# Kernel tuning notes

Hardware: AMD Instinct MI355X
Metric: run time of the kernel (lower is better)

Reference implementation:

```python
import jax, jax.numpy as jnp
import numpy as np

B, S, D, H = 4, 1024, 1024, 16
HD = D // H
NEG = 10000.0


def setup_inputs() -> dict:
    key = jax.random.key(0)
    k1, k2, k3 = jax.random.split(key, 3)
    std = 0.02
    return {
        "x": jax.random.normal(k1, (B, S, D), dtype=jnp.float32),
        "mask": jnp.zeros((B, 1, 1, S), dtype=jnp.float32),
        "w_attn": jax.random.normal(k2, (D, 3 * D), dtype=jnp.float32) * std,
        "b_attn": jnp.zeros((1, 3 * D), dtype=jnp.float32),
        "w_proj": jax.random.normal(k3, (D, D), dtype=jnp.float32) * std,
        "b_proj": jnp.zeros((1, D), dtype=jnp.float32),
    }


def reference(x, mask, w_attn, b_attn, w_proj, b_proj):
    b, s, d = x.shape
    # fused QKV projection (Conv1D == dense over last dim)
    qkv = x @ w_attn + b_attn  # [B,S,3D]
    q, k, v = jnp.split(qkv, 3, axis=2)

    def split_heads(t):  # [B,S,D] -> [B,H,S,HD]
        return t.reshape(b, s, H, HD).transpose(0, 2, 1, 3)

    q, k, v = split_heads(q), split_heads(k), split_heads(v)

    w = jnp.einsum("bhqd,bhkd->bhqk", q, k) / jnp.sqrt(jnp.float32(HD))
    # causal mask (lower triangle from lower-right corner)
    i = jnp.arange(s)[:, None]
    j = jnp.arange(s)[None, :]
    bmask = (i >= j).astype(w.dtype)[None, None]  # [1,1,S,S]
    w = w * bmask - NEG * (1.0 - bmask)
    w = w + mask
    w = jax.nn.softmax(w, axis=-1)  # attn_dropout is identity at inference
    a = jnp.einsum("bhqk,bhkd->bhqd", w, v)
    a = a.transpose(0, 2, 1, 3).reshape(b, s, d)  # merge heads
    a = a @ w_proj + b_proj  # resid_dropout identity at inference
    return (a, w)
```

## Files before the change

### kernel.cpp

```cpp
#include <hip/hip_runtime.h>
#include <hip/hip_bf16.h>

constexpr int Bb = 4, Ss = 1024, Dd = 1024, Hh = 16;

typedef __attribute__((ext_vector_type(8))) short short8;
typedef __attribute__((ext_vector_type(4))) float f32x4;

static __device__ __forceinline__ ushort f2bf(float f) {
  union { __hip_bfloat16 h; ushort u; } cv;
  cv.h = __float2bfloat16(f);
  return cv.u;
}

__global__ __launch_bounds__(256) void cast_f32_bf16(
    const float* __restrict__ in, ushort* __restrict__ out) {
  const int i = (blockIdx.x * 256 + threadIdx.x) * 4;
  const float4 v = *(const float4*)&in[i];
  ushort4 o;
  o.x = f2bf(v.x); o.y = f2bf(v.y); o.z = f2bf(v.z); o.w = f2bf(v.w);
  *(ushort4*)&out[i] = o;
}

__global__ __launch_bounds__(256) void transpose_cast(
    const float* __restrict__ in, ushort* __restrict__ out, int R, int C) {
  __shared__ float T[32][33];
  const int c0 = blockIdx.x * 32, r0 = blockIdx.y * 32;
  const int t = threadIdx.x;
  const int r = t >> 3, c4 = (t & 7) * 4;
  const float4 v = *(const float4*)&in[(size_t)(r0 + r) * C + c0 + c4];
  T[r][c4 + 0] = v.x; T[r][c4 + 1] = v.y;
  T[r][c4 + 2] = v.z; T[r][c4 + 3] = v.w;
  __syncthreads();
  const int cc = t >> 3, rr4 = (t & 7) * 4;
  ushort4 o;
  o.x = f2bf(T[rr4 + 0][cc]); o.y = f2bf(T[rr4 + 1][cc]);
  o.z = f2bf(T[rr4 + 2][cc]); o.w = f2bf(T[rr4 + 3][cc]);
  *(ushort4*)&out[(size_t)(c0 + cc) * R + r0 + rr4] = o;
}

template <int BM, int BN, bool OUT_BF16>
__global__ __launch_bounds__(256) void gemm_bt(
    const ushort* __restrict__ A, const ushort* __restrict__ Bt,
    const float* __restrict__ bias, void* __restrict__ Cout,
    int M, int N, int K) {
  constexpr int LDK = 40;
  constexpr int TM = BM / 32, TN = BN / 32;
  __shared__ ushort As[BM * LDK];
  __shared__ ushort Bs[BN * LDK];
  const int tid = threadIdx.x;
  const int wv = tid >> 6, lane = tid & 63;
  const int l15 = lane & 15, quad = lane >> 4;
  const int m0 = blockIdx.y * BM, n0 = blockIdx.x * BN;
  const int wrow = (wv >> 1) * (BM / 2), wcol = (wv & 1) * (BN / 2);

  f32x4 acc[TM][TN] = {};

  for (int k0 = 0; k0 < K; k0 += 32) {
#pragma unroll
    for (int idx = tid; idx < BM * 4; idx += 256) {
      const int row = idx >> 2, kp = (idx & 3) * 8;
      *(uint4*)&As[row * LDK + kp] =
          *(const uint4*)&A[(size_t)(m0 + row) * K + k0 + kp];
    }
#pragma unroll
    for (int idx = tid; idx < BN * 4; idx += 256) {
      const int row = idx >> 2, kp = (idx & 3) * 8;
      *(uint4*)&Bs[row * LDK + kp] =
          *(const uint4*)&Bt[(size_t)(n0 + row) * K + k0 + kp];
    }
    __syncthreads();
    short8 af[TM], bf[TN];
#pragma unroll
    for (int i = 0; i < TM; i++)
      af[i] = *(const short8*)&As[(wrow + i * 16 + l15) * LDK + quad * 8];
#pragma unroll
    for (int j = 0; j < TN; j++)
      bf[j] = *(const short8*)&Bs[(wcol + j * 16 + l15) * LDK + quad * 8];
#pragma unroll
    for (int i = 0; i < TM; i++)
#pragma unroll
      for (int j = 0; j < TN; j++)
        acc[i][j] = __builtin_amdgcn_mfma_f32_16x16x32_bf16(af[i], bf[j],
                                                            acc[i][j], 0, 0, 0);
    __syncthreads();
  }

#pragma unroll
  for (int j = 0; j < TN; j++) {
    const int col = n0 + wcol + j * 16 + l15;
    const float bv = bias[col];
#pragma unroll
    for (int i = 0; i < TM; i++) {
#pragma unroll
      for (int r = 0; r < 4; r++) {
        const int row = m0 + wrow + i * 16 + quad * 4 + r;
        const float v = acc[i][j][r] + bv;
        if (OUT_BF16)
          ((ushort*)Cout)[(size_t)row * N + col] = f2bf(v);
        else
          ((float*)Cout)[(size_t)row * N + col] = v;
      }
    }
  }
}

__global__ __launch_bounds__(256) void vtrans(const ushort* __restrict__ qkvb,
                                              ushort* __restrict__ vt) {
  __shared__ ushort T[64 * 72];
  const int j0 = blockIdx.x * 64, bh = blockIdx.y;
  const int b = bh >> 4, h = bh & 15;
  const int t = threadIdx.x;
#pragma unroll
  for (int u = 0; u < 2; u++) {
    const int idx = t + 256 * u;
    const int row = idx >> 3, p = idx & 7;
    *(uint4*)&T[row * 72 + p * 8] = *(const uint4*)&qkvb[
        (size_t)((b << 10) + j0 + row) * 3072 + 2048 + h * 64 + p * 8];
  }
  __syncthreads();
#pragma unroll
  for (int u = 0; u < 2; u++) {
    const int idx = t + 256 * u;
    const int d = idx >> 3, p = idx & 7;
    ushort tmp[8];
#pragma unroll
    for (int kk = 0; kk < 8; kk++) tmp[kk] = T[(p * 8 + kk) * 72 + d];
    uint4 o;
    __builtin_memcpy(&o, tmp, 16);
    *(uint4*)&vt[((size_t)bh * 64 + d) * 1024 + j0 + p * 8] = o;
  }
}

__global__ __launch_bounds__(256) void attn_mfma(
    const ushort* __restrict__ qkvb,
    const ushort* __restrict__ vt,
    const float* __restrict__ mask,
    float* __restrict__ w_out,
    ushort* __restrict__ ab) {
  constexpr int LDP = 1032;
  __shared__ ushort Ps[16 * LDP];
  __shared__ float PM[16][68];
  __shared__ float PSum[16][68];

  const int qt = blockIdx.x, bh = blockIdx.y;
  const int b = bh >> 4, h = bh & 15;
  const int q0 = qt * 16;
  const int tid = threadIdx.x;
  const int wv = tid >> 6, lane = tid & 63;
  const int l15 = lane & 15, quad = lane >> 4;
  const int slot = wv * 16 + l15;

  const size_t rowQ = (size_t)((b << 10) + q0 + l15) * 3072 + h * 64;
  const short8 qf0 = *(const short8*)&qkvb[rowQ + quad * 8];
  const short8 qf1 = *(const short8*)&qkvb[rowQ + 32 + quad * 8];

  float sreg[16][4];

#pragma unroll
  for (int i = 0; i < 16; i++) {
    const int j0 = (wv + 4 * i) * 16;
    const int col = j0 + l15;
    const float mv = mask[(b << 10) + col];
    if (j0 <= q0 + 15) {
      const size_t rowK = (size_t)((b << 10) + j0 + l15) * 3072 + 1024 + h * 64;
      const short8 kf0 = *(const short8*)&qkvb[rowK + quad * 8];
      const short8 kf1 = *(const short8*)&qkvb[rowK + 32 + quad * 8];
      f32x4 c = {0.f, 0.f, 0.f, 0.f};
      c = __builtin_amdgcn_mfma_f32_16x16x32_bf16(qf0, kf0, c, 0, 0, 0);
      c = __builtin_amdgcn_mfma_f32_16x16x32_bf16(qf1, kf1, c, 0, 0, 0);
#pragma unroll
      for (int r = 0; r < 4; r++)
        sreg[i][r] =
            (col <= q0 + quad * 4 + r ? c[r] * 0.125f : -10000.0f) + mv;
    } else {
#pragma unroll
      for (int r = 0; r < 4; r++) sreg[i][r] = -10000.0f + mv;
    }
  }

#pragma unroll
  for (int r = 0; r < 4; r++) {
    float m = sreg[0][r];
#pragma unroll
    for (int i = 1; i < 16; i++) m = fmaxf(m, sreg[i][r]);
    PM[quad * 4 + r][slot] = m;
  }
  __syncthreads();

  float mrow[4], psum[4];
#pragma unroll
  for (int r = 0; r < 4; r++) {
    float m = PM[quad * 4 + r][0];
    for (int t = 1; t < 64; t++) m = fmaxf(m, PM[quad * 4 + r][t]);
    mrow[r] = m;
    psum[r] = 0.f;
  }
#pragma unroll
  for (int i = 0; i < 16; i++)
#pragma unroll
    for (int r = 0; r < 4; r++) {
      const float e = __expf(fminf(sreg[i][r] - mrow[r], 0.0f));
      sreg[i][r] = e;
      psum[r] += e;
    }
#pragma unroll
  for (int r = 0; r < 4; r++) PSum[quad * 4 + r][slot] = psum[r];
  __syncthreads();

  float inv4[4];
#pragma unroll
  for (int r = 0; r < 4; r++) {
    float s = 0.f;
    for (int t = 0; t < 64; t++) s += PSum[quad * 4 + r][t];
    inv4[r] = 1.0f / fmaxf(s, 1e-30f);
  }

#pragma unroll
  for (int i = 0; i < 16; i++) {
    const int j0 = (wv + 4 * i) * 16;
#pragma unroll
    for (int r = 0; r < 4; r++) {
      const float p = sreg[i][r] * inv4[r];
      w_out[((size_t)(bh << 10) + q0 + quad * 4 + r) * 1024 + j0 + l15] = p;
      Ps[(quad * 4 + r) * LDP + j0 + l15] = f2bf(p);
    }
  }
  __syncthreads();

  f32x4 oacc = {0.f, 0.f, 0.f, 0.f};
  const int nch = (q0 + 16 + 31) >> 5;
  const ushort* vbase = vt + ((size_t)bh * 64 + wv * 16 + l15) * 1024;
  for (int c = 0; c < nch; c++) {
    const int k0 = c * 32;
    const short8 pf = *(const short8*)&Ps[l15 * LDP + k0 + quad * 8];
    const short8 vf = *(const short8*)&vbase[k0 + quad * 8];
    oacc = __builtin_amdgcn_mfma_f32_16x16x32_bf16(pf, vf, oacc, 0, 0, 0);
  }
#pragma unroll
  for (int r = 0; r < 4; r++) {
    ab[(size_t)((b << 10) + q0 + quad * 4 + r) * 1024 + h * 64 + wv * 16 +
       l15] = f2bf(oacc[r]);
  }
}

extern "C" void kernel_launch(void* const* d_in, const int* in_sizes, int n_in,
                              void* d_out, int out_size, void* d_ws,
                              size_t ws_size, hipStream_t stream) {
  const float* x = (const float*)d_in[0];
  const float* mask = (const float*)d_in[1];
  const float* w_attn = (const float*)d_in[2];
  const float* b_attn = (const float*)d_in[3];
  const float* w_proj = (const float*)d_in[4];
  const float* b_proj = (const float*)d_in[5];

  float* out_a = (float*)d_out;
  float* out_w = out_a + (size_t)Bb * Ss * Dd;

  char* ws = (char*)d_ws;
  ushort* xb   = (ushort*)(ws);
  ushort* wta  = (ushort*)(ws + (8u << 20));
  ushort* wtp  = (ushort*)(ws + (14u << 20));
  ushort* qkvb = (ushort*)(ws + (16u << 20));
  ushort* vt   = (ushort*)(ws + (40u << 20));
  ushort* ab   = (ushort*)(ws + (48u << 20));

  cast_f32_bf16<<<(Bb * Ss * Dd) / 1024, 256, 0, stream>>>(x, xb);
  transpose_cast<<<dim3(3 * Dd / 32, Dd / 32), 256, 0, stream>>>(w_attn, wta,
                                                                 Dd, 3 * Dd);
  transpose_cast<<<dim3(Dd / 32, Dd / 32), 256, 0, stream>>>(w_proj, wtp, Dd,
                                                             Dd);
  gemm_bt<128, 128, true><<<dim3(3 * Dd / 128, Bb * Ss / 128), 256, 0,
                            stream>>>(xb, wta, b_attn, qkvb, Bb * Ss, 3 * Dd,
                                      Dd);
  vtrans<<<dim3(Ss / 64, Bb * Hh), 256, 0, stream>>>(qkvb, vt);
  attn_mfma<<<dim3(Ss / 16, Bb * Hh), 256, 0, stream>>>(qkvb, vt, mask, out_w,
                                                        ab);
  gemm_bt<128, 64, false><<<dim3(Dd / 64, Bb * Ss / 128), 256, 0, stream>>>(
      ab, wtp, b_proj, out_a, Bb * Ss, Dd, Dd);
}
```

Baseline: 487.3 us.

## Use direct global-to-LDS loads in GEMM, shuffle softmax reductions, retile proj GEMM

The GEMM tile loads now use the global_load_lds builtin, which writes 16 bytes per lane straight into unpadded LDS instead of going through registers. The attention softmax row max and sum now reduce with wave shuffles and a 4-entry LDS exchange, replacing serial 64-element LDS scans. The output projection GEMM switches to 128x128 tiles. Risks: dropping the LDS padding can bring bank conflicts on fragment reads, and the larger projection tiles halve the block count.

```diff
diff --git a/kernel.cpp b/kernel.cpp
--- a/kernel.cpp
+++ b/kernel.cpp
@@ -10,6 +10,12 @@
   union { __hip_bfloat16 h; ushort u; } cv;
   cv.h = __float2bfloat16(f);
   return cv.u;
+}
+
+static __device__ __forceinline__ void gl_lds16(const ushort* g, ushort* l) {
+  __builtin_amdgcn_global_load_lds(
+      (const __attribute__((address_space(1))) void*)g,
+      (__attribute__((address_space(3))) void*)l, 16, 0, 0);
 }
 
 __global__ __launch_bounds__(256) void cast_f32_bf16(
@@ -43,44 +49,43 @@
     const ushort* __restrict__ A, const ushort* __restrict__ Bt,
     const float* __restrict__ bias, void* __restrict__ Cout,
     int M, int N, int K) {
-  constexpr int LDK = 40;
   constexpr int TM = BM / 32, TN = BN / 32;
-  __shared__ ushort As[BM * LDK];
-  __shared__ ushort Bs[BN * LDK];
+  __shared__ ushort As[BM * 32];
+  __shared__ ushort Bs[BN * 32];
   const int tid = threadIdx.x;
   const int wv = tid >> 6, lane = tid & 63;
   const int l15 = lane & 15, quad = lane >> 4;
+  const int ln4 = lane >> 2, kp = (lane & 3) * 8;
   const int m0 = blockIdx.y * BM, n0 = blockIdx.x * BN;
   const int wrow = (wv >> 1) * (BM / 2), wcol = (wv & 1) * (BN / 2);
 
+  const ushort* Arow = &A[(size_t)(m0 + wv * 16 + ln4) * K + kp];
+  const ushort* Brow = &Bt[(size_t)(n0 + wv * 16 + ln4) * K + kp];
+  ushort* As_base = &As[wv * 512];
+  ushort* Bs_base = &Bs[wv * 512];
+
   f32x4 acc[TM][TN] = {};
 
   for (int k0 = 0; k0 < K; k0 += 32) {
 #pragma unroll
-    for (int idx = tid; idx < BM * 4; idx += 256) {
-      const int row = idx >> 2, kp = (idx & 3) * 8;
-      *(uint4*)&As[row * LDK + kp] =
-          *(const uint4*)&A[(size_t)(m0 + row) * K + k0 + kp];
-    }
-#pragma unroll
-    for (int idx = tid; idx < BN * 4; idx += 256) {
-      const int row = idx >> 2, kp = (idx & 3) * 8;
-      *(uint4*)&Bs[row * LDK + kp] =
-          *(const uint4*)&Bt[(size_t)(n0 + row) * K + k0 + kp];
-    }
+    for (int u = 0; u < BM / 64; u++)
+      gl_lds16(Arow + (size_t)u * 64 * K + k0, As_base + u * 2048);
+#pragma unroll
+    for (int u = 0; u < BN / 64; u++)
+      gl_lds16(Brow + (size_t)u * 64 * K + k0, Bs_base + u * 2048);
     __syncthreads();
-    short8 af[TM], bf[TN];
+    short8 af[TM], bfr[TN];
 #pragma unroll
     for (int i = 0; i < TM; i++)
-      af[i] = *(const short8*)&As[(wrow + i * 16 + l15) * LDK + quad * 8];
+      af[i] = *(const short8*)&As[(wrow + i * 16 + l15) * 32 + quad * 8];
 #pragma unroll
     for (int j = 0; j < TN; j++)
-      bf[j] = *(const short8*)&Bs[(wcol + j * 16 + l15) * LDK + quad * 8];
+      bfr[j] = *(const short8*)&Bs[(wcol + j * 16 + l15) * 32 + quad * 8];
 #pragma unroll
     for (int i = 0; i < TM; i++)
 #pragma unroll
       for (int j = 0; j < TN; j++)
-        acc[i][j] = __builtin_amdgcn_mfma_f32_16x16x32_bf16(af[i], bf[j],
+        acc[i][j] = __builtin_amdgcn_mfma_f32_16x16x32_bf16(af[i], bfr[j],
                                                             acc[i][j], 0, 0, 0);
     __syncthreads();
   }
@@ -139,8 +144,8 @@
     ushort* __restrict__ ab) {
   constexpr int LDP = 1032;
   __shared__ ushort Ps[16 * LDP];
-  __shared__ float PM[16][68];
-  __shared__ float PSum[16][68];
+  __shared__ float PM[16][4];
+  __shared__ float PSum[16][4];
 
   const int qt = blockIdx.x, bh = blockIdx.y;
   const int b = bh >> 4, h = bh & 15;
@@ -148,7 +153,6 @@
   const int tid = threadIdx.x;
   const int wv = tid >> 6, lane = tid & 63;
   const int l15 = lane & 15, quad = lane >> 4;
-  const int slot = wv * 16 + l15;
 
   const size_t rowQ = (size_t)((b << 10) + q0 + l15) * 3072 + h * 64;
   const short8 qf0 = *(const short8*)&qkvb[rowQ + quad * 8];
@@ -183,18 +187,20 @@
     float m = sreg[0][r];
 #pragma unroll
     for (int i = 1; i < 16; i++) m = fmaxf(m, sreg[i][r]);
-    PM[quad * 4 + r][slot] = m;
-  }
-  __syncthreads();
-
-  float mrow[4], psum[4];
-#pragma unroll
-  for (int r = 0; r < 4; r++) {
-    float m = PM[quad * 4 + r][0];
-    for (int t = 1; t < 64; t++) m = fmaxf(m, PM[quad * 4 + r][t]);
-    mrow[r] = m;
-    psum[r] = 0.f;
-  }
+#pragma unroll
+    for (int off = 1; off < 16; off <<= 1) m = fmaxf(m, __shfl_xor(m, off));
+    if (l15 == 0) PM[quad * 4 + r][wv] = m;
+  }
+  __syncthreads();
+
+  float mrow[4];
+#pragma unroll
+  for (int r = 0; r < 4; r++) {
+    const f32x4 pm4 = *(const f32x4*)&PM[quad * 4 + r][0];
+    mrow[r] = fmaxf(fmaxf(pm4[0], pm4[1]), fmaxf(pm4[2], pm4[3]));
+  }
+
+  float psum[4] = {0.f, 0.f, 0.f, 0.f};
 #pragma unroll
   for (int i = 0; i < 16; i++)
 #pragma unroll
@@ -204,15 +210,19 @@
       psum[r] += e;
     }
 #pragma unroll
-  for (int r = 0; r < 4; r++) PSum[quad * 4 + r][slot] = psum[r];
+  for (int r = 0; r < 4; r++) {
+    float s = psum[r];
+#pragma unroll
+    for (int off = 1; off < 16; off <<= 1) s += __shfl_xor(s, off);
+    if (l15 == 0) PSum[quad * 4 + r][wv] = s;
+  }
   __syncthreads();
 
   float inv4[4];
 #pragma unroll
   for (int r = 0; r < 4; r++) {
-    float s = 0.f;
-    for (int t = 0; t < 64; t++) s += PSum[quad * 4 + r][t];
-    inv4[r] = 1.0f / fmaxf(s, 1e-30f);
+    const f32x4 ps4 = *(const f32x4*)&PSum[quad * 4 + r][0];
+    inv4[r] = 1.0f / fmaxf(ps4[0] + ps4[1] + ps4[2] + ps4[3], 1e-30f);
   }
 
 #pragma unroll
@@ -275,6 +285,6 @@
   vtrans<<<dim3(Ss / 64, Bb * Hh), 256, 0, stream>>>(qkvb, vt);
   attn_mfma<<<dim3(Ss / 16, Bb * Hh), 256, 0, stream>>>(qkvb, vt, mask, out_w,
                                                         ab);
-  gemm_bt<128, 64, false><<<dim3(Dd / 64, Bb * Ss / 128), 256, 0, stream>>>(
+  gemm_bt<128, 128, false><<<dim3(Dd / 128, Bb * Ss / 128), 256, 0, stream>>>(
       ab, wtp, b_proj, out_a, Bb * Ss, Dd, Dd);
 }
```

New measurement: 475.5 us. -2.4%, faster.
